# Performance work log

Hardware: AMD Instinct MI355X
Metric: run time of the kernel (lower is better)

## Reference

```python
import jax, jax.numpy as jnp
import numpy as np
import math

EMBED_DIM = 1024
MEMORY_DIM = 1024
MEMORY_SIZE = 2048
B, S = 8, 4096


def bitnet_linear(x, W, b):
    """Eval-mode BitNetLinear: 1.58-bit weight quant + 8-bit activation quant."""
    w_scale = jnp.mean(jnp.abs(W))
    qW = jnp.sign(W) * (jnp.abs(W) > 0.5 * w_scale).astype(W.dtype)
    i_scale = jnp.max(jnp.abs(x)) / 127.0
    qx = jnp.clip(jnp.round(x / i_scale), -128.0, 127.0)
    out = jnp.einsum('bsi,oi->bso', qx, qW) * (w_scale * i_scale)
    return out + b


def setup_inputs() -> dict:
    key = jax.random.key(0)
    ks = jax.random.split(key, 9)
    return {
        'x': jax.random.normal(ks[0], (B, S, EMBED_DIM), jnp.float32),
        'memory_keys': jax.random.normal(ks[1], (MEMORY_SIZE, MEMORY_DIM), jnp.float32),
        'memory_values': jax.random.normal(ks[2], (MEMORY_SIZE, EMBED_DIM), jnp.float32),
        'Wk': jax.random.normal(ks[3], (MEMORY_DIM, EMBED_DIM), jnp.float32) * 0.1,
        'bk': jnp.zeros((MEMORY_DIM,), jnp.float32),
        'Wv': jax.random.normal(ks[4], (EMBED_DIM, EMBED_DIM), jnp.float32) * 0.1,
        'bv': jnp.zeros((EMBED_DIM,), jnp.float32),
        'Wo': jax.random.normal(ks[5], (EMBED_DIM, EMBED_DIM), jnp.float32) * 0.1,
        'bo': jnp.zeros((EMBED_DIM,), jnp.float32),
    }


def reference(x, memory_keys, memory_values, Wk, bk, Wv, bv, Wo, bo):
    # quantized key/value projections
    query_keys = bitnet_linear(x, Wk, bk)          # [B, S, Dm]
    _query_values = bitnet_linear(x, Wv, bv)       # computed in original (used only by update path)
    # memory cross-attention over fixed bank
    similarities = jnp.einsum('bsd,md->bsm', query_keys, memory_keys)  # [B, S, M]
    attention_weights = jax.nn.softmax(similarities / math.sqrt(MEMORY_DIM), axis=-1)
    retrieved = jnp.einsum('bsm,me->bse', attention_weights, memory_values)  # [B, S, E]
    output = bitnet_linear(x + retrieved, Wo, bo)
    return output
```

## Files before the change

### kernel.cpp

```cpp
#include <hip/hip_runtime.h>
#include <hip/hip_bf16.h>
#include <stdint.h>
#include <type_traits>

typedef __attribute__((ext_vector_type(8))) short bf16x8;
typedef __attribute__((ext_vector_type(4))) float f32x4;
typedef __attribute__((ext_vector_type(4))) int i32x4;

struct Scalars {
  double sum_wk;
  double sum_wo;
  unsigned int max_x_bits;
  unsigned int max_y_bits;
};

__device__ __forceinline__ unsigned short f2bf(float f) {
  __hip_bfloat16 h = __float2bfloat16(f);
  return *reinterpret_cast<unsigned short*>(&h);
}

__device__ __forceinline__ void async16(void* lds, const void* g) {
  __builtin_amdgcn_global_load_lds((__attribute__((address_space(1))) void*)g,
                                   (__attribute__((address_space(3))) void*)lds, 16, 0, 0);
}

__device__ __forceinline__ void tile_swizzle(int nxShift, int& bx, int& by) {
  const int per = gridDim.x >> 3;
  const int tile = (blockIdx.x & 7) * per + (blockIdx.x >> 3);
  bx = tile & ((1 << nxShift) - 1);
  by = tile >> nxShift;
}

__device__ __forceinline__ f32x4 mm(bf16x8 a, bf16x8 b, f32x4 c) {
  return __builtin_amdgcn_mfma_f32_16x16x32_bf16(a, b, c, 0, 0, 0);
}
__device__ __forceinline__ i32x4 mm(i32x4 a, i32x4 b, i32x4 c) {
  return __builtin_amdgcn_mfma_i32_16x16x64_i8(a, b, c, 0, 0, 0);
}

__global__ __launch_bounds__(256) void stats_kernel(const float* __restrict__ Wk,
                                                    const float* __restrict__ Wo,
                                                    const float* __restrict__ x,
                                                    Scalars* __restrict__ sc) {
  const int which = blockIdx.y;
  size_t tid = (size_t)blockIdx.x * 256 + threadIdx.x;
  size_t stride = (size_t)gridDim.x * 256;
  if (which < 2) {
    const float* w = which ? Wo : Wk;
    const size_t n = 1048576;
    double s = 0.0;
    for (size_t i = tid * 4; i < n; i += stride * 4) {
      float4 v = *(const float4*)(w + i);
      s += (double)fabsf(v.x) + (double)fabsf(v.y) + (double)fabsf(v.z) + (double)fabsf(v.w);
    }
#pragma unroll
    for (int o = 32; o > 0; o >>= 1) s += __shfl_xor(s, o);
    __shared__ double sm[4];
    if ((threadIdx.x & 63) == 0) sm[threadIdx.x >> 6] = s;
    __syncthreads();
    if (threadIdx.x == 0)
      atomicAdd(which ? &sc->sum_wo : &sc->sum_wk, sm[0] + sm[1] + sm[2] + sm[3]);
  } else {
    const size_t n = (size_t)32768 * 1024;
    float m = 0.0f;
    for (size_t i = tid * 4; i < n; i += stride * 4) {
      float4 v = *(const float4*)(x + i);
      m = fmaxf(m, fmaxf(fmaxf(fabsf(v.x), fabsf(v.y)), fmaxf(fabsf(v.z), fabsf(v.w))));
    }
#pragma unroll
    for (int o = 32; o > 0; o >>= 1) m = fmaxf(m, __shfl_xor(m, o));
    __shared__ float smf[4];
    if ((threadIdx.x & 63) == 0) smf[threadIdx.x >> 6] = m;
    __syncthreads();
    if (threadIdx.x == 0)
      atomicMax(&sc->max_x_bits,
                __float_as_uint(fmaxf(fmaxf(smf[0], smf[1]), fmaxf(smf[2], smf[3]))));
  }
}

__global__ __launch_bounds__(256) void prep_kernel(
    const float* __restrict__ Wk, const float* __restrict__ Wo,
    const float* __restrict__ mk, const float* __restrict__ mv,
    const float* __restrict__ x, char* __restrict__ qWk8, char* __restrict__ qWo8,
    __hip_bfloat16* __restrict__ mkb, __hip_bfloat16* __restrict__ mvT,
    char* __restrict__ qx8, const Scalars* __restrict__ sc) {
  __shared__ float tl[32][33];
  const int which = blockIdx.y;
  const int t = threadIdx.x;
  size_t tid = (size_t)blockIdx.x * 256 + t;
  size_t stride = (size_t)gridDim.x * 256;
  if (which < 2) {
    const float* W = which ? Wo : Wk;
    char* q = which ? qWo8 : qWk8;
    const double sum = which ? sc->sum_wo : sc->sum_wk;
    const float thr = 0.5f * (float)(sum * (1.0 / 1048576.0));
    const size_t n = 1048576;
    for (size_t i = tid * 4; i < n; i += stride * 4) {
      float4 v = *(const float4*)(W + i);
      char4 o;
      o.x = (char)(fabsf(v.x) > thr ? (v.x > 0.f ? 1 : -1) : 0);
      o.y = (char)(fabsf(v.y) > thr ? (v.y > 0.f ? 1 : -1) : 0);
      o.z = (char)(fabsf(v.z) > thr ? (v.z > 0.f ? 1 : -1) : 0);
      o.w = (char)(fabsf(v.w) > thr ? (v.w > 0.f ? 1 : -1) : 0);
      *(char4*)(q + i) = o;
    }
  } else if (which == 2) {
    const size_t n = (size_t)2048 * 1024;
    for (size_t i = tid * 4; i < n; i += stride * 4) {
      float4 v = *(const float4*)(mk + i);
      ushort4 o;
      o.x = f2bf(v.x); o.y = f2bf(v.y); o.z = f2bf(v.z); o.w = f2bf(v.w);
      *(ushort4*)((unsigned short*)mkb + i) = o;
    }
  } else if (which == 3) {
    const int ti = blockIdx.x & 31;
    const int tj = blockIdx.x >> 5;
    const int tx = t & 31, ty = t >> 5;
#pragma unroll
    for (int r = 0; r < 4; ++r)
      tl[ty + r * 8][tx] = mv[(size_t)(tj * 32 + ty + r * 8) * 1024 + ti * 32 + tx];
    __syncthreads();
#pragma unroll
    for (int r = 0; r < 4; ++r)
      mvT[(size_t)(ti * 32 + ty + r * 8) * 2048 + tj * 32 + tx] =
          __float2bfloat16(tl[tx][ty + r * 8]);
  } else {
    const float isc = __uint_as_float(sc->max_x_bits) / 127.0f;
    const size_t n = (size_t)32768 * 1024;
    for (size_t i = tid * 4; i < n; i += stride * 4) {
      float4 v = *(const float4*)(x + i);
      char4 o;
      o.x = (char)(int)fminf(fmaxf(rintf(v.x / isc), -128.f), 127.f);
      o.y = (char)(int)fminf(fmaxf(rintf(v.y / isc), -128.f), 127.f);
      o.z = (char)(int)fminf(fmaxf(rintf(v.z / isc), -128.f), 127.f);
      o.w = (char)(int)fminf(fmaxf(rintf(v.w / isc), -128.f), 127.f);
      *(char4*)(qx8 + i) = o;
    }
  }
}

__global__ __launch_bounds__(256) void quant_act_bf16_kernel(
    const __hip_bfloat16* __restrict__ y, char* __restrict__ q,
    const unsigned int* __restrict__ maxbits, size_t n) {
  const float isc = __uint_as_float(*maxbits) / 127.0f;
  size_t tid = (size_t)blockIdx.x * blockDim.x + threadIdx.x;
  size_t stride = (size_t)gridDim.x * blockDim.x;
  for (size_t i = tid * 8; i < n; i += stride * 8) {
    uint4 r = *(const uint4*)((const unsigned short*)y + i);
    float v[8];
    v[0] = __uint_as_float(r.x << 16); v[1] = __uint_as_float(r.x & 0xffff0000u);
    v[2] = __uint_as_float(r.y << 16); v[3] = __uint_as_float(r.y & 0xffff0000u);
    v[4] = __uint_as_float(r.z << 16); v[5] = __uint_as_float(r.z & 0xffff0000u);
    v[6] = __uint_as_float(r.w << 16); v[7] = __uint_as_float(r.w & 0xffff0000u);
    char o[8];
#pragma unroll
    for (int j = 0; j < 8; ++j)
      o[j] = (char)(int)fminf(fmaxf(rintf(v[j] / isc), -128.f), 127.f);
    uint2 pk;
    pk.x = (unsigned char)o[0] | ((unsigned)(unsigned char)o[1] << 8) |
           ((unsigned)(unsigned char)o[2] << 16) | ((unsigned)(unsigned char)o[3] << 24);
    pk.y = (unsigned char)o[4] | ((unsigned)(unsigned char)o[5] << 8) |
           ((unsigned)(unsigned char)o[6] << 16) | ((unsigned)(unsigned char)o[7] << 24);
    *(uint2*)(q + i) = pk;
  }
}

__global__ __launch_bounds__(256) void softmax_kernel(__hip_bfloat16* __restrict__ sims) {
  const int t = threadIdx.x, l = t & 63, wv = t >> 6;
  unsigned short* row = (unsigned short*)(sims + ((size_t)blockIdx.x * 4 + wv) * 2048);
  uint4 r4[4];
  float v[32];
#pragma unroll
  for (int c = 0; c < 4; ++c) r4[c] = *(const uint4*)(row + c * 512 + l * 8);
#pragma unroll
  for (int c = 0; c < 4; ++c) {
    unsigned u0 = r4[c].x, u1 = r4[c].y, u2 = r4[c].z, u3 = r4[c].w;
    v[c * 8 + 0] = __uint_as_float(u0 << 16); v[c * 8 + 1] = __uint_as_float(u0 & 0xffff0000u);
    v[c * 8 + 2] = __uint_as_float(u1 << 16); v[c * 8 + 3] = __uint_as_float(u1 & 0xffff0000u);
    v[c * 8 + 4] = __uint_as_float(u2 << 16); v[c * 8 + 5] = __uint_as_float(u2 & 0xffff0000u);
    v[c * 8 + 6] = __uint_as_float(u3 << 16); v[c * 8 + 7] = __uint_as_float(u3 & 0xffff0000u);
  }
  float m = v[0];
#pragma unroll
  for (int i = 1; i < 32; ++i) m = fmaxf(m, v[i]);
#pragma unroll
  for (int o = 32; o > 0; o >>= 1) m = fmaxf(m, __shfl_xor(m, o));
  float s = 0.f;
#pragma unroll
  for (int i = 0; i < 32; ++i) { v[i] = expf(v[i] - m); s += v[i]; }
#pragma unroll
  for (int o = 32; o > 0; o >>= 1) s += __shfl_xor(s, o);
#pragma unroll
  for (int c = 0; c < 4; ++c) {
    unsigned short b[8];
#pragma unroll
    for (int j = 0; j < 8; ++j) b[j] = f2bf(v[c * 8 + j] / s);
    uint4 o4;
    o4.x = (unsigned)b[0] | ((unsigned)b[1] << 16);
    o4.y = (unsigned)b[2] | ((unsigned)b[3] << 16);
    o4.z = (unsigned)b[4] | ((unsigned)b[5] << 16);
    o4.w = (unsigned)b[6] | ((unsigned)b[7] << 16);
    *(uint4*)(row + c * 512 + l * 8) = o4;
  }
}

#define CFENCE() asm volatile("" ::: "memory")
#define BAR8() { CFENCE(); __builtin_amdgcn_s_barrier(); CFENCE(); }
#define WLGKM(N) { asm volatile("s_waitcnt lgkmcnt(" #N ")" ::: "memory"); __builtin_amdgcn_sched_barrier(0); }
#define WVM(N) asm volatile("s_waitcnt vmcnt(" #N ")" ::: "memory")

template <int EPI>
__global__ __launch_bounds__(512, 2) void gemm8(
    const char* __restrict__ A, const char* __restrict__ B, void* __restrict__ C,
    const float* __restrict__ aux, Scalars* __restrict__ sc,
    int Ndim, int KB, int nxShift) {
  constexpr bool I8 = (EPI >= 3);
  using FR  = typename std::conditional<I8, i32x4, bf16x8>::type;
  using ACC = typename std::conditional<I8, i32x4, f32x4>::type;
  __shared__ __align__(16) char lds[4][2][16384];

  int bx, by;
  tile_swizzle(nxShift, bx, by);
  const int rowBlk = by * 256, colBlk = bx * 256;

  const int t = threadIdx.x, w = t >> 6, l = t & 63;
  const int wm = w >> 2, wn = w & 3;
  const int quad = l >> 4, m16 = l & 15;
  const int NT = KB >> 7, NIT = NT >> 1;

  int voA[2][2], voB[2][2];
#pragma unroll
  for (int hf = 0; hf < 2; ++hf)
#pragma unroll
    for (int j = 0; j < 2; ++j) {
      const int idx = j * 64 + (t >> 3);
      const int kby = ((t & 7) ^ (idx & 7)) << 4;
      voA[hf][j] = (rowBlk + ((idx >> 6) << 7) + (hf << 6) + (idx & 63)) * KB + kby;
      voB[hf][j] = (colBlk + ((idx >> 5) << 6) + (hf << 5) + (idx & 31)) * KB + kby;
    }

  const char* baA[2];
  const char* baB[2];
#pragma unroll
  for (int ks = 0; ks < 2; ++ks) {
    const int x16 = ((ks << 6) + (quad << 4)) ^ ((m16 & 7) << 4);
    baA[ks] = &lds[0][0][(wm * 64 + m16) * 128 + x16];
    baB[ks] = &lds[2][0][(wn * 32 + m16) * 128 + x16];
  }

#define STG_A(slot, hf, tk)                                                         \
  if ((tk) < NT) {                                                                  \
    _Pragma("unroll") for (int j = 0; j < 2; ++j)                                   \
      async16(&lds[hf][slot][j * 8192 + (w << 10)],                                 \
              A + (((size_t)(tk)) << 7) + voA[hf][j]);                              \
  }
#define STG_B(slot, hf, tk)                                                         \
  if ((tk) < NT) {                                                                  \
    _Pragma("unroll") for (int j = 0; j < 2; ++j)                                   \
      async16(&lds[2 + (hf)][slot][j * 8192 + (w << 10)],                           \
              B + (((size_t)(tk)) << 7) + voB[hf][j]);                              \
  }

#define LD_A(dst, slot, hf, f, ks) \
  dst = *(const FR*)(baA[ks] + ((hf)*32768 + (slot)*16384 + (f)*2048));
#define LD_B(dst, slot, hf, gg, ks) \
  dst = *(const FR*)(baB[ks] + ((hf)*32768 + (slot)*16384 + (gg)*2048));

#define R_A0(s) { _Pragma("unroll") for (int f_ = 0; f_ < 4; ++f_) { LD_A(af[f_][0], s, 0, f_, 0); LD_A(af[f_][1], s, 0, f_, 1); } }
#define R_A1(s) { _Pragma("unroll") for (int f_ = 0; f_ < 4; ++f_) { LD_A(af[f_][0], s, 1, f_, 0); LD_A(af[f_][1], s, 1, f_, 1); } }
#define R_B0(s) { _Pragma("unroll") for (int g_ = 0; g_ < 2; ++g_) { LD_B(b0[g_][0], s, 0, g_, 0); LD_B(b0[g_][1], s, 0, g_, 1); } }
#define R_B1(s) { _Pragma("unroll") for (int g_ = 0; g_ < 2; ++g_) { LD_B(b1[g_][0], s, 1, g_, 0); LD_B(b1[g_][1], s, 1, g_, 1); } }

#define MM8(FO, GO, BR)                                                             \
  __builtin_amdgcn_s_setprio(1);                                                    \
  _Pragma("unroll") for (int f_ = 0; f_ < 4; ++f_)                                  \
    _Pragma("unroll") for (int g_ = 0; g_ < 2; ++g_) {                              \
      acc[(FO) + f_][(GO) + g_] = mm(af[f_][0], BR[g_][0], acc[(FO) + f_][(GO) + g_]); \
      acc[(FO) + f_][(GO) + g_] = mm(af[f_][1], BR[g_][1], acc[(FO) + f_][(GO) + g_]); \
    }                                                                               \
  __builtin_amdgcn_s_setprio(0);

#define TSTEP(s, tk, last)                                                          \
  {                                                                                 \
    R_B1(s);                                                                        \
    STG_A((s) ^ 1, 1, (tk) + 1);                                                    \
    BAR8(); WLGKM(4);                                                               \
    MM8(0, 0, b0);                                                                  \
    BAR8();                                                                         \
    STG_A(s, 0, (tk) + 2);                                                          \
    BAR8(); WLGKM(0);                                                               \
    MM8(0, 2, b1);                                                                  \
    R_A1(s);                                                                        \
    BAR8();                                                                         \
    STG_B(s, 0, (tk) + 2);                                                          \
    BAR8(); WLGKM(0);                                                               \
    MM8(4, 0, b0);                                                                  \
    BAR8();                                                                         \
    STG_B(s, 1, (tk) + 2);                                                          \
    if (last) { WVM(0); } else { WVM(6); }                                          \
    BAR8();                                                                         \
    MM8(4, 2, b1);                                                                  \
    R_A0((s) ^ 1);                                                                  \
    R_B0((s) ^ 1);                                                                  \
  }

  FR af[4][2], b0[2][2], b1[2][2];
  ACC acc[8][4] = {};

  STG_A(0, 0, 0); STG_B(0, 0, 0); STG_B(0, 1, 0); STG_A(0, 1, 0);
  CFENCE();
  STG_A(1, 0, 1); STG_B(1, 0, 1); STG_B(1, 1, 1);
  WVM(6);
  BAR8();
  R_A0(0); R_B0(0);

  for (int it = 0; it < NIT; ++it) {
    const bool last = (it == NIT - 1);
    TSTEP(0, it * 2, last);
    TSTEP(1, it * 2 + 1, last);
  }

  float sK = 0.0f;
  if constexpr (EPI == 3)
    sK = (float)(sc->sum_wk * (1.0 / 1048576.0)) * (__uint_as_float(sc->max_x_bits) / 127.0f);
  if constexpr (EPI == 4)
    sK = (float)(sc->sum_wo * (1.0 / 1048576.0)) * (__uint_as_float(sc->max_y_bits) / 127.0f);

  float amax = 0.0f;
#pragma unroll
  for (int f = 0; f < 8; ++f) {
#pragma unroll
    for (int g = 0; g < 4; ++g) {
      const int col = colBlk + wn * 64 + g * 16 + m16;
#pragma unroll
      for (int rg = 0; rg < 4; ++rg) {
        const int row = rowBlk + wm * 128 + f * 16 + quad * 4 + rg;
        if constexpr (EPI == 1) {
          ((__hip_bfloat16*)C)[(size_t)row * Ndim + col] =
              __float2bfloat16(acc[f][g][rg] * 0.03125f);
        } else if constexpr (EPI == 2) {
          float v = acc[f][g][rg] + aux[(size_t)row * Ndim + col];
          ((__hip_bfloat16*)C)[(size_t)row * Ndim + col] = __float2bfloat16(v);
          amax = fmaxf(amax, fabsf(v));
        } else if constexpr (EPI == 3) {
          ((__hip_bfloat16*)C)[(size_t)row * Ndim + col] =
              __float2bfloat16((float)acc[f][g][rg] * sK + aux[col]);
        } else {
          ((float*)C)[(size_t)row * Ndim + col] = (float)acc[f][g][rg] * sK + aux[col];
        }
      }
    }
  }

  if constexpr (EPI == 2) {
#pragma unroll
    for (int o = 32; o > 0; o >>= 1) amax = fmaxf(amax, __shfl_xor(amax, o));
    if (l == 0) atomicMax(&sc->max_y_bits, __float_as_uint(amax));
  }
#undef STG_A
#undef STG_B
#undef LD_A
#undef LD_B
#undef R_A0
#undef R_A1
#undef R_B0
#undef R_B1
#undef MM8
#undef TSTEP
}

extern "C" void kernel_launch(void* const* d_in, const int* in_sizes, int n_in,
                              void* d_out, int out_size, void* d_ws, size_t ws_size,
                              hipStream_t stream) {
  (void)in_sizes; (void)n_in; (void)out_size; (void)ws_size;
  const float* x  = (const float*)d_in[0];
  const float* mk = (const float*)d_in[1];
  const float* mv = (const float*)d_in[2];
  const float* Wk = (const float*)d_in[3];
  const float* bk = (const float*)d_in[4];
  const float* Wo = (const float*)d_in[7];
  const float* bo = (const float*)d_in[8];
  float* out = (float*)d_out;

  const int M = 32768, E = 1024, MEM = 2048;

  char* ws = (char*)d_ws;
  Scalars* sc = (Scalars*)ws;
  const size_t off0 = 256;
  char* qx8 = ws + off0;
  __hip_bfloat16* qk = (__hip_bfloat16*)(ws + off0 + (size_t)M * E);
  __hip_bfloat16* yb = (__hip_bfloat16*)(ws + off0);
  const size_t off1 = off0 + (size_t)M * E * 4;
  __hip_bfloat16* sims = (__hip_bfloat16*)(ws + off1);
  char* qy8 = (char*)sims;
  const size_t off2 = off1 + (size_t)M * MEM * 2;
  char* qWk8 = ws + off2;
  char* qWo8 = qWk8 + (size_t)E * E;
  __hip_bfloat16* mkb = (__hip_bfloat16*)(qWo8 + (size_t)E * E);
  __hip_bfloat16* mvT = mkb + (size_t)MEM * E;

  hipMemsetAsync(ws, 0, 256, stream);

  stats_kernel<<<dim3(1024, 3), dim3(256), 0, stream>>>(Wk, Wo, x, sc);
  prep_kernel<<<dim3(2048, 5), dim3(256), 0, stream>>>(Wk, Wo, mk, mv, x, qWk8, qWo8,
                                                       mkb, mvT, qx8, sc);

  gemm8<3><<<dim3((E / 256) * (M / 256)), dim3(512), 0, stream>>>(
      qx8, qWk8, qk, bk, sc, E, E, 2);
  gemm8<1><<<dim3((MEM / 256) * (M / 256)), dim3(512), 0, stream>>>(
      (const char*)qk, (const char*)mkb, sims, nullptr, sc, MEM, 2 * E, 3);
  softmax_kernel<<<dim3(M / 4), dim3(256), 0, stream>>>(sims);
  gemm8<2><<<dim3((E / 256) * (M / 256)), dim3(512), 0, stream>>>(
      (const char*)sims, (const char*)mvT, yb, x, sc, E, 2 * MEM, 2);
  quant_act_bf16_kernel<<<dim3(2048), dim3(256), 0, stream>>>(yb, qy8, &sc->max_y_bits,
                                                              (size_t)M * E);
  gemm8<4><<<dim3((E / 256) * (M / 256)), dim3(512), 0, stream>>>(
      qy8, qWo8, out, bo, sc, E, E, 2);
}
```

Measured before the change: 760.9 us.

## Fold quantized key projection into memory keys to skip the 32k-row int8 GEMM

Reassociates the similarity computation so the quantized Wk projection is applied to the 2048-row memory key bank instead of the 32768 activations. A small bf16 GEMM builds K2 = mk·qWkᵀ·scale, and the bias term bk·mk becomes a per-column bias added in the similarity epilogue. The large int8 x·Wk GEMM and the qk intermediate buffer go away, and the similarity GEMM now reads bf16 quantized x directly. In exchange, quantized x is stored as bf16 (twice the bytes of int8), and K2 rounding to bf16 changes numerics slightly.

```diff
diff --git a/kernel.cpp b/kernel.cpp
--- a/kernel.cpp
+++ b/kernel.cpp
@@ -41,6 +41,9 @@
 __global__ __launch_bounds__(256) void stats_kernel(const float* __restrict__ Wk,
                                                     const float* __restrict__ Wo,
                                                     const float* __restrict__ x,
+                                                    const float* __restrict__ bk,
+                                                    const float* __restrict__ mk,
+                                                    float* __restrict__ bias2,
                                                     Scalars* __restrict__ sc) {
   const int which = blockIdx.y;
   size_t tid = (size_t)blockIdx.x * 256 + threadIdx.x;
@@ -60,7 +63,7 @@
     __syncthreads();
     if (threadIdx.x == 0)
       atomicAdd(which ? &sc->sum_wo : &sc->sum_wk, sm[0] + sm[1] + sm[2] + sm[3]);
-  } else {
+  } else if (which == 2) {
     const size_t n = (size_t)32768 * 1024;
     float m = 0.0f;
     for (size_t i = tid * 4; i < n; i += stride * 4) {
@@ -75,34 +78,63 @@
     if (threadIdx.x == 0)
       atomicMax(&sc->max_x_bits,
                 __float_as_uint(fmaxf(fmaxf(smf[0], smf[1]), fmaxf(smf[2], smf[3]))));
+  } else {
+    if (blockIdx.x >= 512) return;
+    const int l = threadIdx.x & 63, wv = threadIdx.x >> 6;
+    const int m = blockIdx.x * 4 + wv;
+    float dot = 0.f;
+#pragma unroll
+    for (int c = 0; c < 4; ++c) {
+      float4 b4 = *(const float4*)(bk + c * 256 + l * 4);
+      float4 k4 = *(const float4*)(mk + (size_t)m * 1024 + c * 256 + l * 4);
+      dot += b4.x * k4.x + b4.y * k4.y + b4.z * k4.z + b4.w * k4.w;
+    }
+#pragma unroll
+    for (int o = 32; o > 0; o >>= 1) dot += __shfl_xor(dot, o);
+    if (l == 0) bias2[m] = dot * 0.03125f;
   }
 }
 
 __global__ __launch_bounds__(256) void prep_kernel(
     const float* __restrict__ Wk, const float* __restrict__ Wo,
     const float* __restrict__ mk, const float* __restrict__ mv,
-    const float* __restrict__ x, char* __restrict__ qWk8, char* __restrict__ qWo8,
-    __hip_bfloat16* __restrict__ mkb, __hip_bfloat16* __restrict__ mvT,
-    char* __restrict__ qx8, const Scalars* __restrict__ sc) {
+    const float* __restrict__ x, __hip_bfloat16* __restrict__ qWkT,
+    char* __restrict__ qWo8, __hip_bfloat16* __restrict__ mkb,
+    __hip_bfloat16* __restrict__ mvT, __hip_bfloat16* __restrict__ qxb,
+    const Scalars* __restrict__ sc) {
   __shared__ float tl[32][33];
   const int which = blockIdx.y;
   const int t = threadIdx.x;
   size_t tid = (size_t)blockIdx.x * 256 + t;
   size_t stride = (size_t)gridDim.x * 256;
-  if (which < 2) {
-    const float* W = which ? Wo : Wk;
-    char* q = which ? qWo8 : qWk8;
-    const double sum = which ? sc->sum_wo : sc->sum_wk;
+  if (which == 0) {
+    if (blockIdx.x >= 1024) return;
+    const float thr = 0.5f * (float)(sc->sum_wk * (1.0 / 1048576.0));
+    const int ti = blockIdx.x & 31;
+    const int tj = blockIdx.x >> 5;
+    const int tx = t & 31, ty = t >> 5;
+#pragma unroll
+    for (int r = 0; r < 4; ++r)
+      tl[ty + r * 8][tx] = Wk[(size_t)(tj * 32 + ty + r * 8) * 1024 + ti * 32 + tx];
+    __syncthreads();
+#pragma unroll
+    for (int r = 0; r < 4; ++r) {
+      float v = tl[tx][ty + r * 8];
+      float q = fabsf(v) > thr ? (v > 0.f ? 1.f : -1.f) : 0.f;
+      qWkT[(size_t)(ti * 32 + ty + r * 8) * 1024 + tj * 32 + tx] = __float2bfloat16(q);
+    }
+  } else if (which == 1) {
+    const double sum = sc->sum_wo;
     const float thr = 0.5f * (float)(sum * (1.0 / 1048576.0));
     const size_t n = 1048576;
     for (size_t i = tid * 4; i < n; i += stride * 4) {
-      float4 v = *(const float4*)(W + i);
+      float4 v = *(const float4*)(Wo + i);
       char4 o;
       o.x = (char)(fabsf(v.x) > thr ? (v.x > 0.f ? 1 : -1) : 0);
       o.y = (char)(fabsf(v.y) > thr ? (v.y > 0.f ? 1 : -1) : 0);
       o.z = (char)(fabsf(v.z) > thr ? (v.z > 0.f ? 1 : -1) : 0);
       o.w = (char)(fabsf(v.w) > thr ? (v.w > 0.f ? 1 : -1) : 0);
-      *(char4*)(q + i) = o;
+      *(char4*)(qWo8 + i) = o;
     }
   } else if (which == 2) {
     const size_t n = (size_t)2048 * 1024;
@@ -129,12 +161,12 @@
     const size_t n = (size_t)32768 * 1024;
     for (size_t i = tid * 4; i < n; i += stride * 4) {
       float4 v = *(const float4*)(x + i);
-      char4 o;
-      o.x = (char)(int)fminf(fmaxf(rintf(v.x / isc), -128.f), 127.f);
-      o.y = (char)(int)fminf(fmaxf(rintf(v.y / isc), -128.f), 127.f);
-      o.z = (char)(int)fminf(fmaxf(rintf(v.z / isc), -128.f), 127.f);
-      o.w = (char)(int)fminf(fmaxf(rintf(v.w / isc), -128.f), 127.f);
-      *(char4*)(qx8 + i) = o;
+      ushort4 o;
+      o.x = f2bf(fminf(fmaxf(rintf(v.x / isc), -128.f), 127.f));
+      o.y = f2bf(fminf(fmaxf(rintf(v.y / isc), -128.f), 127.f));
+      o.z = f2bf(fminf(fmaxf(rintf(v.z / isc), -128.f), 127.f));
+      o.w = f2bf(fminf(fmaxf(rintf(v.w / isc), -128.f), 127.f));
+      *(ushort4*)((unsigned short*)qxb + i) = o;
     }
   }
 }
@@ -214,7 +246,7 @@
     const char* __restrict__ A, const char* __restrict__ B, void* __restrict__ C,
     const float* __restrict__ aux, Scalars* __restrict__ sc,
     int Ndim, int KB, int nxShift) {
-  constexpr bool I8 = (EPI >= 3);
+  constexpr bool I8 = (EPI == 4);
   using FR  = typename std::conditional<I8, i32x4, bf16x8>::type;
   using ACC = typename std::conditional<I8, i32x4, f32x4>::type;
   __shared__ __align__(16) char lds[4][2][16384];
@@ -321,8 +353,9 @@
   }
 
   float sK = 0.0f;
-  if constexpr (EPI == 3)
-    sK = (float)(sc->sum_wk * (1.0 / 1048576.0)) * (__uint_as_float(sc->max_x_bits) / 127.0f);
+  if constexpr (EPI == 5)
+    sK = (float)(sc->sum_wk * (1.0 / 1048576.0)) *
+         (__uint_as_float(sc->max_x_bits) / 127.0f) * 0.03125f;
   if constexpr (EPI == 4)
     sK = (float)(sc->sum_wo * (1.0 / 1048576.0)) * (__uint_as_float(sc->max_y_bits) / 127.0f);
 
@@ -337,14 +370,14 @@
         const int row = rowBlk + wm * 128 + f * 16 + quad * 4 + rg;
         if constexpr (EPI == 1) {
           ((__hip_bfloat16*)C)[(size_t)row * Ndim + col] =
-              __float2bfloat16(acc[f][g][rg] * 0.03125f);
+              __float2bfloat16(acc[f][g][rg] + aux[col]);
         } else if constexpr (EPI == 2) {
           float v = acc[f][g][rg] + aux[(size_t)row * Ndim + col];
           ((__hip_bfloat16*)C)[(size_t)row * Ndim + col] = __float2bfloat16(v);
           amax = fmaxf(amax, fabsf(v));
-        } else if constexpr (EPI == 3) {
+        } else if constexpr (EPI == 5) {
           ((__hip_bfloat16*)C)[(size_t)row * Ndim + col] =
-              __float2bfloat16((float)acc[f][g][rg] * sK + aux[col]);
+              __float2bfloat16(acc[f][g][rg] * sK);
         } else {
           ((float*)C)[(size_t)row * Ndim + col] = (float)acc[f][g][rg] * sK + aux[col];
         }
@@ -387,33 +420,34 @@
   char* ws = (char*)d_ws;
   Scalars* sc = (Scalars*)ws;
   const size_t off0 = 256;
-  char* qx8 = ws + off0;
-  __hip_bfloat16* qk = (__hip_bfloat16*)(ws + off0 + (size_t)M * E);
-  __hip_bfloat16* yb = (__hip_bfloat16*)(ws + off0);
-  const size_t off1 = off0 + (size_t)M * E * 4;
+  __hip_bfloat16* qxb = (__hip_bfloat16*)(ws + off0);
+  __hip_bfloat16* yb  = (__hip_bfloat16*)(ws + off0);
+  const size_t off1 = off0 + (size_t)M * E * 2;
   __hip_bfloat16* sims = (__hip_bfloat16*)(ws + off1);
   char* qy8 = (char*)sims;
   const size_t off2 = off1 + (size_t)M * MEM * 2;
-  char* qWk8 = ws + off2;
-  char* qWo8 = qWk8 + (size_t)E * E;
+  __hip_bfloat16* qWkT = (__hip_bfloat16*)(ws + off2);
+  char* qWo8 = (char*)(qWkT + (size_t)E * E);
   __hip_bfloat16* mkb = (__hip_bfloat16*)(qWo8 + (size_t)E * E);
   __hip_bfloat16* mvT = mkb + (size_t)MEM * E;
+  __hip_bfloat16* K2b = mvT + (size_t)E * MEM;
+  float* bias2 = (float*)(K2b + (size_t)MEM * E);
 
   hipMemsetAsync(ws, 0, 256, stream);
 
-  stats_kernel<<<dim3(1024, 3), dim3(256), 0, stream>>>(Wk, Wo, x, sc);
-  prep_kernel<<<dim3(2048, 5), dim3(256), 0, stream>>>(Wk, Wo, mk, mv, x, qWk8, qWo8,
-                                                       mkb, mvT, qx8, sc);
-
-  gemm8<3><<<dim3((E / 256) * (M / 256)), dim3(512), 0, stream>>>(
-      qx8, qWk8, qk, bk, sc, E, E, 2);
+  stats_kernel<<<dim3(1024, 4), dim3(256), 0, stream>>>(Wk, Wo, x, bk, mk, bias2, sc);
+  prep_kernel<<<dim3(2048, 5), dim3(256), 0, stream>>>(Wk, Wo, mk, mv, x, qWkT, qWo8,
+                                                       mkb, mvT, qxb, sc);
+
+  gemm8<5><<<dim3((E / 256) * (MEM / 256)), dim3(512), 0, stream>>>(
+      (const char*)mkb, (const char*)qWkT, K2b, nullptr, sc, E, 2 * E, 2);
   gemm8<1><<<dim3((MEM / 256) * (M / 256)), dim3(512), 0, stream>>>(
-      (const char*)qk, (const char*)mkb, sims, nullptr, sc, MEM, 2 * E, 3);
+      (const char*)qxb, (const char*)K2b, sims, bias2, sc, MEM, 2 * E, 3);
   softmax_kernel<<<dim3(M / 4), dim3(256), 0, stream>>>(sims);
   gemm8<2><<<dim3((E / 256) * (M / 256)), dim3(512), 0, stream>>>(
       (const char*)sims, (const char*)mvT, yb, x, sc, E, 2 * MEM, 2);
   quant_act_bf16_kernel<<<dim3(2048), dim3(256), 0, stream>>>(yb, qy8, &sc->max_y_bits,
                                                               (size_t)M * E);
   gemm8<4><<<dim3((E / 256) * (M / 256)), dim3(512), 0, stream>>>(
-      qy8, qWo8, out, bo, sc, E, E, 2);
-}
+      (const char*)qy8, (const char*)qWo8, out, bo, sc, E, E, 2);
+}
```

Result: faster. 737.7 us (-3.1%).
